# Kernel optimization log

Measured on AMD Instinct MI355X. Metric: run time of the kernel, lower is better.

Reference implementation:

```python
import jax, jax.numpy as jnp
import numpy as np

B, T, E, H = 4, 2048, 1024, 16
HD = E // H

def setup_inputs() -> dict:
    key = jax.random.key(0)
    ks = jax.random.split(key, 5)
    s = 1.0 / np.sqrt(E)
    return {
        "x": jax.random.normal(ks[0], (B, T, E), dtype=jnp.float32),
        "mask": jnp.zeros((B, T), dtype=bool),
        "qkv_w": jax.random.uniform(ks[1], (3 * E, E), jnp.float32, -s, s),
        "qkv_b": jax.random.uniform(ks[2], (3 * E,), jnp.float32, -s, s),
        "proj_w": jax.random.uniform(ks[3], (E, E), jnp.float32, -s, s),
        "proj_b": jax.random.uniform(ks[4], (E,), jnp.float32, -s, s),
    }

def reference(x, mask, qkv_w, qkv_b, proj_w, proj_b):
    b, t, e = x.shape
    qkv = x @ qkv_w.T + qkv_b                      # [b,t,3e]
    q, k, v = jnp.split(qkv, 3, axis=2)
    # [b,t,e] -> [b,h,t,hd]
    q = q.reshape(b, t, H, HD).transpose(0, 2, 1, 3)
    k = k.reshape(b, t, H, HD).transpose(0, 2, 1, 3)
    v = v.reshape(b, t, H, HD).transpose(0, 2, 1, 3)
    scale = 1.0 / np.sqrt(HD)
    attn = jnp.einsum('bhqd,bhkd->bhqk', q, k) * scale
    # mask: True -> -inf, broadcast over heads and query positions
    neg = jnp.where(mask, -jnp.inf, 0.0).astype(attn.dtype)  # [b,t]
    attn = attn + neg[:, None, None, :]
    attn = jax.nn.softmax(attn, axis=-1)
    # dropout layers in eval mode (deterministic reference)
    out = jnp.einsum('bhqk,bhkd->bhqd', attn, v)   # [b,h,t,hd]
    out = out.transpose(0, 2, 1, 3).reshape(b, t, e)
    return out @ proj_w.T + proj_b
```

## Files before the change

kernel.cpp:

```cpp
#include <hip/hip_runtime.h>
#include <stdint.h>

#define Bz  4
#define Tz  2048
#define Ez  1024
#define Hz  16
#define HDz 64
#define Mz  (Bz*Tz)

typedef short bf16x8 __attribute__((ext_vector_type(8)));
typedef float f32x4  __attribute__((ext_vector_type(4)));
typedef unsigned short u16;

__device__ __forceinline__ u16 f2bf(float f) {
  return (u16)((__builtin_bit_cast(uint32_t, f) + 0x8000u) >> 16);
}
__device__ __forceinline__ uint32_t pack2bf(float a, float b) {
  uint32_t ua = __builtin_bit_cast(uint32_t, a) + 0x8000u;
  uint32_t ub = __builtin_bit_cast(uint32_t, b) + 0x8000u;
  return __builtin_amdgcn_perm(ub, ua, 0x07060302u);
}
__device__ __forceinline__ uint32_t cvtpk2bf(float a, float b) {
  uint32_t r;
  asm("v_cvt_pk_bf16_f32 %0, %1, %2" : "=v"(r) : "v"(a), "v"(b));
  return r;
}

#if __has_builtin(__builtin_amdgcn_exp2f)
#define EXP2(x) __builtin_amdgcn_exp2f(x)
#else
#define EXP2(x) exp2f(x)
#endif

__device__ __forceinline__ void gl2lds16(const u16* g, u16* l) {
  __builtin_amdgcn_global_load_lds((const __attribute__((address_space(1))) void*)g,
                                   (__attribute__((address_space(3))) void*)l, 16, 0, 0);
}

__global__ void cvt_f32_bf16_3(const float* __restrict__ s0, u16* __restrict__ d0, int n0,
                               const float* __restrict__ s1, u16* __restrict__ d1, int n1,
                               const float* __restrict__ s2, u16* __restrict__ d2, int n2) {
  int j = blockIdx.x * blockDim.x + threadIdx.x;
  const float* s; u16* d;
  if (j < n0) { s = s0; d = d0; }
  else {
    j -= n0;
    if (j < n1) { s = s1; d = d1; }
    else { j -= n1; if (j >= n2) return; s = s2; d = d2; }
  }
  float4 f = ((const float4*)s)[j];
  uint2 o;
  o.x = pack2bf(f.x, f.y);
  o.y = pack2bf(f.z, f.w);
  ((uint2*)d)[j] = o;
}

template<int MODE>
__global__ __launch_bounds__(256, 2) void gemm_bt(
    const u16* __restrict__ A, const u16* __restrict__ Bw,
    const float* __restrict__ bias,
    u16* __restrict__ qo, u16* __restrict__ ko, u16* __restrict__ vto,
    float* __restrict__ fo)
{
  __shared__ u16 Ab[2][128*64];
  __shared__ u16 Bb[2][128*64];
  const int tid  = threadIdx.x;
  const int lane = tid & 63;
  const int wid  = tid >> 6;
  const int quad = lane >> 4;
  const int cl   = lane & 15;
  const int wm   = wid >> 1, wn = wid & 1;
  const int bm   = blockIdx.y * 128;
  const int bn   = blockIdx.x * 128;
  const int srow = lane >> 3;
  const int ssw  = lane & 7;

  f32x4 acc[4][4] = {};

  auto stage = [&](int kt, int buf) {
#pragma unroll
    for (int s = 0; s < 4; ++s) {
      const int r  = wid*32 + s*8 + srow;
      const int cc = ssw ^ (r & 7);
      gl2lds16(A + (size_t)(bm + r)*Ez + kt + cc*8, &Ab[buf][(wid*32 + s*8)*64]);
    }
#pragma unroll
    for (int s = 0; s < 4; ++s) {
      const int r  = wid*32 + s*8 + srow;
      const int cc = ssw ^ (r & 7);
      gl2lds16(Bw + (size_t)(bn + r)*Ez + kt + cc*8, &Bb[buf][(wid*32 + s*8)*64]);
    }
  };

  stage(0, 0);

#pragma unroll 2
  for (int it = 0; it < 16; ++it) {
    const int bufc = it & 1;
    __syncthreads();
    if (it < 15) stage((it+1)*64, bufc^1);
    const u16* AB = &Ab[bufc][0];
    const u16* BB = &Bb[bufc][0];
#pragma unroll
    for (int ks = 0; ks < 2; ++ks) {
      bf16x8 af[4], bfr[4];
#pragma unroll
      for (int mi = 0; mi < 4; ++mi) {
        const int row = wm*64 + mi*16 + cl;
        const int ch  = (ks*4 + quad) ^ (row & 7);
        af[mi] = *(const bf16x8*)&AB[row*64 + ch*8];
      }
#pragma unroll
      for (int ni = 0; ni < 4; ++ni) {
        const int row = wn*64 + ni*16 + cl;
        const int ch  = (ks*4 + quad) ^ (row & 7);
        bfr[ni] = *(const bf16x8*)&BB[row*64 + ch*8];
      }
#pragma unroll
      for (int mi = 0; mi < 4; ++mi)
#pragma unroll
        for (int ni = 0; ni < 4; ++ni)
          acc[mi][ni] = __builtin_amdgcn_mfma_f32_16x16x32_bf16(af[mi], bfr[ni], acc[mi][ni], 0, 0, 0);
    }
  }

  const float qsc = 0.125f * 1.4426950408889634f;
#pragma unroll
  for (int ni = 0; ni < 4; ++ni) {
    const int n   = bn + wn*64 + ni*16 + cl;
    const float bv = bias[n];
#pragma unroll
    for (int mi = 0; mi < 4; ++mi) {
      const int m0 = bm + wm*64 + mi*16 + quad*4;
      if (MODE == 0) {
        const int which = n >> 10;
        const int e = n & 1023;
        const int h = e >> 6, d = e & 63;
        const int b = m0 >> 11, t0 = m0 & 2047;
        if (which == 2) {
          uint2 pk;
          pk.x = pack2bf(acc[mi][ni][0] + bv, acc[mi][ni][1] + bv);
          pk.y = pack2bf(acc[mi][ni][2] + bv, acc[mi][ni][3] + bv);
          *(uint2*)&vto[(((size_t)(b*Hz + h))*HDz + d)*Tz + t0] = pk;
        } else {
#pragma unroll
          for (int r = 0; r < 4; ++r) {
            const int t = t0 + r;
            float val = acc[mi][ni][r] + bv;
            if (which == 0) qo[(((size_t)(b*Hz + h))*Tz + t)*HDz + d] = f2bf(val * qsc);
            else            ko[(((size_t)(b*Hz + h))*Tz + t)*HDz + d] = f2bf(val);
          }
        }
      } else {
#pragma unroll
        for (int r = 0; r < 4; ++r)
          fo[(size_t)(m0 + r)*Ez + n] = acc[mi][ni][r] + bv;
      }
    }
  }
}

__global__ __launch_bounds__(256, 4) void attn_flash(
    const u16* __restrict__ Q, const u16* __restrict__ K,
    const u16* __restrict__ Vt, const unsigned char* __restrict__ mask,
    u16* __restrict__ ctx)
{
  __shared__ u16 Kb[2][64*64];
  __shared__ u16 Vb[2][64*64];

  const int tid  = threadIdx.x;
  const int lane = tid & 63;
  const int wid  = tid >> 6;
  const int quad = lane >> 4;
  const int cl   = lane & 15;
  const int bh   = blockIdx.x;
  const int b    = bh >> 4;
  const int qrw  = blockIdx.y * 128 + wid * 32;

  const int srow = wid*16 + (lane >> 3);
  const int sch  = (lane & 7) ^ (srow & 7);
  const u16* Kg = K  + ((size_t)bh*Tz + srow)*HDz + sch*8;
  const u16* Vg = Vt + ((size_t)bh*HDz + srow)*Tz + sch*8;
  u16* KbL[2] = { &Kb[0][(wid*16)*64], &Kb[1][(wid*16)*64] };
  u16* VbL[2] = { &Vb[0][(wid*16)*64], &Vb[1][(wid*16)*64] };

  auto stage = [&](int kt, int buf) {
    gl2lds16(Kg + (size_t)kt*HDz,           KbL[buf]);
    gl2lds16(Kg + (size_t)kt*HDz + 8*HDz,   KbL[buf] + 8*64);
    gl2lds16(Vg + kt,                       VbL[buf]);
    gl2lds16(Vg + kt + (size_t)8*Tz,        VbL[buf] + 8*64);
  };

  const unsigned char* mrow_p = mask + (size_t)b * Tz;
  bool domask;
  {
    const uint4* mp = (const uint4*)mrow_p;
    uint4 a = mp[lane*2], c = mp[lane*2 + 1];
    uint32_t any = a.x | a.y | a.z | a.w | c.x | c.y | c.z | c.w;
    domask = __any(any != 0);
  }

  bf16x8 aq[2][2];
#pragma unroll
  for (int qb = 0; qb < 2; ++qb) {
    const u16* Qg = Q + ((size_t)bh*Tz + qrw + qb*16 + cl)*HDz;
    aq[qb][0] = *(const bf16x8*)(Qg + quad*8);
    aq[qb][1] = *(const bf16x8*)(Qg + 32 + quad*8);
  }

  bf16x8 ones;
#pragma unroll
  for (int i = 0; i < 8; ++i) ones[i] = (short)0x3F80;

  f32x4 o[2][4] = {};
  f32x4 lacc[2] = {};

  stage(0, 0);

#pragma unroll 2
  for (int it = 0; it < 32; ++it) {
    const int bufc = it & 1;
    __syncthreads();
    if (it < 31) stage((it+1)*64, bufc^1);
    const u16* KB = &Kb[bufc][0];
    const u16* VB = &Vb[bufc][0];
    const int kt = it * 64;

#pragma unroll
    for (int kv = 0; kv < 2; ++kv) {
      f32x4 st[2][2] = {};
#pragma unroll
      for (int kb = 0; kb < 2; ++kb) {
        bf16x8 kf[2];
#pragma unroll
        for (int nb = 0; nb < 2; ++nb) {
          const int row = kv*32 + nb*16 + cl;
          const int ch  = (kb*4 + quad) ^ (row & 7);
          kf[nb] = *(const bf16x8*)&KB[row*64 + ch*8];
        }
#pragma unroll
        for (int qb = 0; qb < 2; ++qb)
#pragma unroll
          for (int nb = 0; nb < 2; ++nb)
            st[qb][nb] = __builtin_amdgcn_mfma_f32_16x16x32_bf16(kf[nb], aq[qb][kb], st[qb][nb], 0, 0, 0);
      }

      if (domask) {
#pragma unroll
        for (int nb = 0; nb < 2; ++nb) {
          uint32_t mm = *(const uint32_t*)&mrow_p[kt + kv*32 + nb*16 + quad*4];
          if (mm) {
#pragma unroll
            for (int qb = 0; qb < 2; ++qb) {
              if (mm & 0x000000ffu) st[qb][nb][0] = -INFINITY;
              if (mm & 0x0000ff00u) st[qb][nb][1] = -INFINITY;
              if (mm & 0x00ff0000u) st[qb][nb][2] = -INFINITY;
              if (mm & 0xff000000u) st[qb][nb][3] = -INFINITY;
            }
          }
        }
      }

      bf16x8 pf[2];
#pragma unroll
      for (int qb = 0; qb < 2; ++qb) {
        uint32_t ux = cvtpk2bf(EXP2(st[qb][0][0]), EXP2(st[qb][0][1]));
        uint32_t uy = cvtpk2bf(EXP2(st[qb][0][2]), EXP2(st[qb][0][3]));
        uint32_t vx = cvtpk2bf(EXP2(st[qb][1][0]), EXP2(st[qb][1][1]));
        uint32_t vy = cvtpk2bf(EXP2(st[qb][1][2]), EXP2(st[qb][1][3]));
        asm("v_permlane32_swap_b32 %0, %1" : "+v"(ux), "+v"(vx));
        asm("v_permlane32_swap_b32 %0, %1" : "+v"(uy), "+v"(vy));
        asm("v_permlane16_swap_b32 %0, %1" : "+v"(ux), "+v"(vx));
        asm("v_permlane16_swap_b32 %0, %1" : "+v"(uy), "+v"(vy));
        int4 pi = { (int)ux, (int)uy, (int)vx, (int)vy };
        pf[qb] = __builtin_bit_cast(bf16x8, pi);
        lacc[qb] = __builtin_amdgcn_mfma_f32_16x16x32_bf16(pf[qb], ones, lacc[qb], 0, 0, 0);
      }

#pragma unroll
      for (int db = 0; db < 4; ++db) {
        const int row = db*16 + cl;
        const int ch  = (kv*4 + quad) ^ (row & 7);
        bf16x8 bv = *(const bf16x8*)&VB[row*64 + ch*8];
#pragma unroll
        for (int qb = 0; qb < 2; ++qb)
          o[qb][db] = __builtin_amdgcn_mfma_f32_16x16x32_bf16(pf[qb], bv, o[qb][db], 0, 0, 0);
      }
    }
  }

#pragma unroll
  for (int qb = 0; qb < 2; ++qb) {
#pragma unroll
    for (int r = 0; r < 4; ++r) {
      const float inv = 1.0f / lacc[qb][r];
      const int t = qrw + qb*16 + quad*4 + r;
      const size_t base = ((size_t)b*Tz + t)*Ez + (size_t)(bh & 15)*HDz;
#pragma unroll
      for (int db = 0; db < 4; ++db) {
        ctx[base + db*16 + cl] = f2bf(o[qb][db][r] * inv);
      }
    }
  }
}

extern "C" void kernel_launch(void* const* d_in, const int* in_sizes, int n_in,
                              void* d_out, int out_size, void* d_ws, size_t ws_size,
                              hipStream_t stream) {
  (void)in_sizes; (void)n_in; (void)out_size; (void)ws_size;
  const float* x      = (const float*)d_in[0];
  const unsigned char* mask = (const unsigned char*)d_in[1];
  const float* qkv_w  = (const float*)d_in[2];
  const float* qkv_b  = (const float*)d_in[3];
  const float* proj_w = (const float*)d_in[4];
  const float* proj_b = (const float*)d_in[5];
  float* out = (float*)d_out;

  char* ws = (char*)d_ws;
  u16* xb   = (u16*)(ws + 0);
  u16* wqb  = (u16*)(ws + 16777216);
  u16* wpb  = (u16*)(ws + 23068672);
  u16* Qb   = (u16*)(ws + 25165824);
  u16* Kb_  = (u16*)(ws + 41943040);
  u16* Vtb  = (u16*)(ws + 58720256);
  u16* ctxb = (u16*)(ws + 75497472);

  cvt_f32_bf16_3<<<12288, 256, 0, stream>>>(x, xb, 2097152,
                                            qkv_w, wqb, 786432,
                                            proj_w, wpb, 262144);

  gemm_bt<0><<<dim3(24, 64), 256, 0, stream>>>(xb, wqb, qkv_b, Qb, Kb_, Vtb, nullptr);
  attn_flash<<<dim3(64, 16), 256, 0, stream>>>(Qb, Kb_, Vtb, mask, ctxb);
  gemm_bt<1><<<dim3(8, 64), 256, 0, stream>>>(ctxb, wpb, proj_b, nullptr, nullptr, nullptr, out);
}
```

Baseline: 256.2 us.

## Use 256x128 GEMM tiles with 8 waves and a triple-buffered LDS pipeline

The GEMM block tile grows from 128x128 with 4 waves to 256x128 with 8 waves, so each B tile is reused across twice as many rows. LDS staging becomes a 3-deep ring with explicit vmcnt waits and raw barriers, keeping two tiles of loads in flight instead of one. MFMA sections are raised to higher priority with s_setprio. This costs more LDS per block (about 144KB), which may limit occupancy to one block per CU. The hand-written vmcnt counts also depend on the exact number of async loads issued per stage.

Result: no change. 253.9 us (-0.9%).

```diff
diff --git a/kernel.cpp b/kernel.cpp
--- a/kernel.cpp
+++ b/kernel.cpp
@@ -56,51 +56,58 @@
 }
 
 template<int MODE>
-__global__ __launch_bounds__(256, 2) void gemm_bt(
+__global__ __launch_bounds__(512, 2) void gemm_bt(
     const u16* __restrict__ A, const u16* __restrict__ Bw,
     const float* __restrict__ bias,
     u16* __restrict__ qo, u16* __restrict__ ko, u16* __restrict__ vto,
     float* __restrict__ fo)
 {
-  __shared__ u16 Ab[2][128*64];
-  __shared__ u16 Bb[2][128*64];
+  __shared__ u16 Lds[3][(256 + 128) * 64];
   const int tid  = threadIdx.x;
   const int lane = tid & 63;
   const int wid  = tid >> 6;
   const int quad = lane >> 4;
   const int cl   = lane & 15;
-  const int wm   = wid >> 1, wn = wid & 1;
-  const int bm   = blockIdx.y * 128;
+  const int wm   = wid >> 1;
+  const int wn   = wid & 1;
+  const int bm   = blockIdx.y * 256;
   const int bn   = blockIdx.x * 128;
-  const int srow = lane >> 3;
-  const int ssw  = lane & 7;
+  const int srow8 = lane >> 3;
+  const int sch   = lane & 7;
 
   f32x4 acc[4][4] = {};
 
-  auto stage = [&](int kt, int buf) {
+  auto stage = [&](int t, int buf) {
+    const int kt = t * 64;
+    u16* base = &Lds[buf][0];
 #pragma unroll
     for (int s = 0; s < 4; ++s) {
-      const int r  = wid*32 + s*8 + srow;
-      const int cc = ssw ^ (r & 7);
-      gl2lds16(A + (size_t)(bm + r)*Ez + kt + cc*8, &Ab[buf][(wid*32 + s*8)*64]);
-    }
-#pragma unroll
-    for (int s = 0; s < 4; ++s) {
-      const int r  = wid*32 + s*8 + srow;
-      const int cc = ssw ^ (r & 7);
-      gl2lds16(Bw + (size_t)(bn + r)*Ez + kt + cc*8, &Bb[buf][(wid*32 + s*8)*64]);
+      const int r  = s*64 + wid*8 + srow8;
+      const int cc = sch ^ (r & 7);
+      gl2lds16(A + (size_t)(bm + r)*Ez + kt + cc*8, base + (s*64 + wid*8)*64);
+    }
+#pragma unroll
+    for (int s = 0; s < 2; ++s) {
+      const int r  = s*64 + wid*8 + srow8;
+      const int cc = sch ^ (r & 7);
+      gl2lds16(Bw + (size_t)(bn + r)*Ez + kt + cc*8, base + (256*64) + (s*64 + wid*8)*64);
     }
   };
 
   stage(0, 0);
-
-#pragma unroll 2
-  for (int it = 0; it < 16; ++it) {
-    const int bufc = it & 1;
-    __syncthreads();
-    if (it < 15) stage((it+1)*64, bufc^1);
-    const u16* AB = &Ab[bufc][0];
-    const u16* BB = &Bb[bufc][0];
+  stage(1, 1);
+
+#pragma unroll
+  for (int t = 0; t < 16; ++t) {
+    const int buf = t % 3;
+    if (t + 2 < 16) stage(t + 2, (t + 2) % 3);
+    if (t < 14)       asm volatile("s_waitcnt vmcnt(12)" ::: "memory");
+    else if (t == 14) asm volatile("s_waitcnt vmcnt(6)"  ::: "memory");
+    else              asm volatile("s_waitcnt vmcnt(0)"  ::: "memory");
+    __builtin_amdgcn_s_barrier();
+    __builtin_amdgcn_sched_barrier(0);
+    const u16* AB = &Lds[buf][0];
+    const u16* BB = &Lds[buf][256*64];
 #pragma unroll
     for (int ks = 0; ks < 2; ++ks) {
       bf16x8 af[4], bfr[4];
@@ -116,12 +123,15 @@
         const int ch  = (ks*4 + quad) ^ (row & 7);
         bfr[ni] = *(const bf16x8*)&BB[row*64 + ch*8];
       }
+      __builtin_amdgcn_s_setprio(1);
 #pragma unroll
       for (int mi = 0; mi < 4; ++mi)
 #pragma unroll
         for (int ni = 0; ni < 4; ++ni)
           acc[mi][ni] = __builtin_amdgcn_mfma_f32_16x16x32_bf16(af[mi], bfr[ni], acc[mi][ni], 0, 0, 0);
-    }
+      __builtin_amdgcn_s_setprio(0);
+    }
+    __builtin_amdgcn_s_barrier();
   }
 
   const float qsc = 0.125f * 1.4426950408889634f;
@@ -329,7 +339,7 @@
                                             qkv_w, wqb, 786432,
                                             proj_w, wpb, 262144);
 
-  gemm_bt<0><<<dim3(24, 64), 256, 0, stream>>>(xb, wqb, qkv_b, Qb, Kb_, Vtb, nullptr);
+  gemm_bt<0><<<dim3(24, 32), 512, 0, stream>>>(xb, wqb, qkv_b, Qb, Kb_, Vtb, nullptr);
   attn_flash<<<dim3(64, 16), 256, 0, stream>>>(Qb, Kb_, Vtb, mask, ctxb);
-  gemm_bt<1><<<dim3(8, 64), 256, 0, stream>>>(ctxb, wpb, proj_b, nullptr, nullptr, nullptr, out);
-}
+  gemm_bt<1><<<dim3(8, 32), 512, 0, stream>>>(ctxb, wpb, proj_b, nullptr, nullptr, nullptr, out);
+}
```
